# Performance work log

Measured on AMD Instinct MI355X. Metric: run time of the kernel, lower is better.

Reference implementation:

```python
import jax, jax.numpy as jnp
import numpy as np


def _gcn_conv(x, W, b, src, dst, num_nodes):
    """PyG GCNConv: linear transform, add self-loops, symmetric norm, scatter-add."""
    h = x @ W  # [N, out] - transform first (cheaper gather on small dim)
    loop = jnp.arange(num_nodes, dtype=src.dtype)
    s = jnp.concatenate([src, loop])  # sources (message senders)
    d = jnp.concatenate([dst, loop])  # targets (aggregators)
    deg = jax.ops.segment_sum(jnp.ones_like(d, dtype=h.dtype), d, num_segments=num_nodes)
    dinv = jnp.where(deg > 0, jax.lax.rsqrt(deg), 0.0)
    norm = dinv[s] * dinv[d]  # [E+N]
    msg = h[s] * norm[:, None]  # gather + scale
    out = jax.ops.segment_sum(msg, d, num_segments=num_nodes)  # scatter-add
    return out + b


def setup_inputs() -> dict:
    key = jax.random.key(0)
    k1, k2, k3, k4 = jax.random.split(key, 4)
    N, F_IN, H, C, E = 100000, 128, 16, 7, 3200000
    x = jax.random.normal(k1, (N, F_IN), dtype=jnp.float32)
    edge_index = jax.random.randint(k2, (2, E), 0, N, dtype=jnp.int64)
    W1 = jax.random.normal(k3, (F_IN, H), dtype=jnp.float32) / np.sqrt(F_IN)
    b1 = jnp.zeros((H,), dtype=jnp.float32)
    W2 = jax.random.normal(k4, (H, C), dtype=jnp.float32) / np.sqrt(H)
    b2 = jnp.zeros((C,), dtype=jnp.float32)
    return {"x": x, "edge_index": edge_index, "W1": W1, "b1": b1, "W2": W2, "b2": b2}


def reference(x, edge_index, W1, b1, W2, b2):
    N = x.shape[0]
    src, dst = edge_index[0], edge_index[1]
    h = _gcn_conv(x, W1, b1, src, dst, N)
    h = jax.nn.relu(h)
    # dropout is identity in eval mode
    h = _gcn_conv(h, W2, b2, src, dst, N)
    return jax.nn.log_softmax(h, axis=1)
```

## Files before the change

### kernel.cpp

```cpp
#include <hip/hip_runtime.h>

#define BSHIFT 7
#define BNODES 128
#define BMASK 127
#define CAP 6144
#define PT 512
#define P_EPB (PT * 16)
#define TPB 256

__device__ __forceinline__ unsigned pkbf2(float a, float b) {
    unsigned ua = __float_as_uint(a), ub = __float_as_uint(b);
    ua = (ua + 0x7fffu + ((ua >> 16) & 1u)) >> 16;
    ub = (ub + 0x7fffu + ((ub >> 16) & 1u)) >> 16;
    return ua | (ub << 16);
}
__device__ __forceinline__ float bflo(unsigned u) { return __uint_as_float(u << 16); }
__device__ __forceinline__ float bfhi(unsigned u) { return __uint_as_float(u & 0xffff0000u); }

__global__ void detect_kernel(const unsigned int* __restrict__ w, int* __restrict__ flag,
                              int* __restrict__ gcur, int nb) {
    __shared__ int any;
    if (threadIdx.x == 0) any = 0;
    __syncthreads();
    int nz = 0;
    for (int k = threadIdx.x; k < 1024; k += blockDim.x)
        if (w[2 * k + 1] != 0u) nz = 1;
    if (nz) atomicOr(&any, 1);
    for (int i = threadIdx.x; i < nb; i += blockDim.x) gcur[i] = 0;
    __syncthreads();
    if (threadIdx.x == 0) *flag = (any == 0) ? 1 : 0;
}

__global__ __launch_bounds__(PT) void fused_place_gemm_kernel(
    const void* __restrict__ ei, const int* __restrict__ flag,
    int* __restrict__ gcur, unsigned* __restrict__ pairs,
    const float* __restrict__ x, const float* __restrict__ W1,
    uint4* __restrict__ hs1u, int E, int nb, int pb, int N) {
    __shared__ alignas(16) char smem[47120];
    int tid = threadIdx.x;
    if ((int)blockIdx.x < pb) {
        int* cnt  = (int*)smem;
        int* bbs  = (int*)(smem + 4096);
        int* cur  = (int*)(smem + 8208);
        int* ssum = (int*)(smem + 12304);
        unsigned* stage = (unsigned*)(smem + 14352);
        const bool is64 = (*flag != 0);
        const long long* e64 = (const long long*)ei;
        const int* e32 = (const int*)ei;
        int e0 = blockIdx.x * P_EPB;
        int tot = E - e0; if (tot > P_EPB) tot = P_EPB;
        for (int b = tid; b < nb; b += PT) cnt[b] = 0;
        __syncthreads();
        unsigned pk[16];
        int bk[16];
#pragma unroll
        for (int k = 0; k < 16; ++k) {
            int i = tid + k * PT;
            bk[k] = -1;
            if (i < tot) {
                int e = e0 + i;
                int s, d;
                if (is64) { s = (int)e64[e]; d = (int)e64[E + e]; }
                else      { s = e32[e];      d = e32[E + e]; }
                int b = d >> BSHIFT;
                bk[k] = b;
                pk[k] = ((unsigned)s << BSHIFT) | (unsigned)(d & BMASK);
                atomicAdd(&cnt[b], 1);
            }
        }
        __syncthreads();
        int t2 = tid * 2;
        int c0 = (t2 < nb) ? cnt[t2] : 0;
        int c1 = (t2 + 1 < nb) ? cnt[t2 + 1] : 0;
        int ts = c0 + c1;
        ssum[tid] = ts;
        __syncthreads();
        for (int off = 1; off < PT; off <<= 1) {
            int v = (tid >= off) ? ssum[tid - off] : 0;
            __syncthreads();
            ssum[tid] += v;
            __syncthreads();
        }
        int excl = ssum[tid] - ts;
        if (tid == PT - 1) bbs[nb] = ssum[PT - 1];
        int gb0 = 0, gb1 = 0;
        if (t2 < nb && c0) gb0 = atomicAdd(&gcur[t2], c0);
        if (t2 + 1 < nb && c1) gb1 = atomicAdd(&gcur[t2 + 1], c1);
        if (t2 < nb)     { bbs[t2] = excl;          cnt[t2] = gb0;     cur[t2] = 0; }
        if (t2 + 1 < nb) { bbs[t2 + 1] = excl + c0; cnt[t2 + 1] = gb1; cur[t2 + 1] = 0; }
        __syncthreads();
#pragma unroll
        for (int k = 0; k < 16; ++k) {
            if (bk[k] >= 0) {
                int r = atomicAdd(&cur[bk[k]], 1);
                stage[bbs[bk[k]] + r] = pk[k];
            }
        }
        __syncthreads();
        for (int i = tid; i < tot; i += PT) {
            int lo = 0, hi = nb;
            while (hi - lo > 1) { int mid = (lo + hi) >> 1; if (bbs[mid] <= i) lo = mid; else hi = mid; }
            int slot = cnt[lo] + (i - bbs[lo]);
            if (slot < CAP) pairs[(size_t)lo * CAP + slot] = stage[i];
        }
    } else {
        float* Ws = (float*)smem;
        for (int i = tid; i < 2048; i += PT) Ws[i] = W1[i];
        __syncthreads();
        int n = ((int)blockIdx.x - pb) * PT + tid;
        if (n >= N) return;
        const float4* xp = (const float4*)(x + (size_t)n * 128);
        float a[16];
#pragma unroll
        for (int j = 0; j < 16; ++j) a[j] = 0.f;
#pragma unroll 4
        for (int k4 = 0; k4 < 32; ++k4) {
            float4 xv = xp[k4];
            const float* wr = &Ws[k4 * 64];
#pragma unroll
            for (int j = 0; j < 16; ++j) a[j] += xv.x * wr[j];
#pragma unroll
            for (int j = 0; j < 16; ++j) a[j] += xv.y * wr[16 + j];
#pragma unroll
            for (int j = 0; j < 16; ++j) a[j] += xv.z * wr[32 + j];
#pragma unroll
            for (int j = 0; j < 16; ++j) a[j] += xv.w * wr[48 + j];
        }
        uint4 u0, u1;
        u0.x = pkbf2(a[0], a[1]);   u0.y = pkbf2(a[2], a[3]);
        u0.z = pkbf2(a[4], a[5]);   u0.w = pkbf2(a[6], a[7]);
        u1.x = pkbf2(a[8], a[9]);   u1.y = pkbf2(a[10], a[11]);
        u1.z = pkbf2(a[12], a[13]); u1.w = pkbf2(a[14], a[15]);
        hs1u[(size_t)n * 2]     = u0;
        hs1u[(size_t)n * 2 + 1] = u1;
    }
}

__global__ __launch_bounds__(TPB) void csr_build_kernel(
    const unsigned* __restrict__ pairs, const int* __restrict__ gcur,
    int* __restrict__ csr, int* __restrict__ row, int* __restrict__ degA,
    const uint4* __restrict__ hs1u, uint4* __restrict__ hs1b, int N) {
    __shared__ int hist[BNODES];
    __shared__ int sc[BNODES];
    __shared__ int cur[BNODES];
    __shared__ int stage[CAP];
    int tid = threadIdx.x;
    int b = blockIdx.x;
    if (tid < BNODES) hist[tid] = 0;
    __syncthreads();
    int cnt = gcur[b]; if (cnt > CAP) cnt = CAP;
    int base = b * CAP;
    const unsigned* sl = pairs + (size_t)b * CAP;
    for (int i = tid; i < cnt; i += TPB)
        atomicAdd(&hist[sl[i] & BMASK], 1);
    __syncthreads();
    if (tid < BNODES) sc[tid] = hist[tid];
    __syncthreads();
    for (int off = 1; off < BNODES; off <<= 1) {
        int u = (tid < BNODES && tid >= off) ? sc[tid - off] : 0;
        __syncthreads();
        if (tid < BNODES) sc[tid] += u;
        __syncthreads();
    }
    if (tid < BNODES) {
        int excl = sc[tid] - hist[tid];
        sc[tid] = excl;
        cur[tid] = 0;
        int node = (b << BSHIFT) + tid;
        if (node < N) {
            row[node]  = base + excl;
            degA[node] = hist[tid];
        }
    }
    __syncthreads();
    for (int i = tid; i < cnt; i += TPB) {
        unsigned val = sl[i];
        int l = val & BMASK;
        int r = atomicAdd(&cur[l], 1);
        stage[sc[l] + r] = (int)(val >> BSHIFT);
    }
    __syncthreads();
    for (int i = tid; i < cnt; i += TPB)
        csr[base + i] = stage[i];
    {
        int ln = tid >> 1, half = tid & 1;
        int node = (b << BSHIFT) + ln;
        if (node < N) {
            float s = rsqrtf((float)(hist[ln] + 1));
            uint4 uu = hs1u[(size_t)node * 2 + half];
            uint4 o;
            o.x = pkbf2(bflo(uu.x) * s, bfhi(uu.x) * s);
            o.y = pkbf2(bflo(uu.y) * s, bfhi(uu.y) * s);
            o.z = pkbf2(bflo(uu.z) * s, bfhi(uu.z) * s);
            o.w = pkbf2(bflo(uu.w) * s, bfhi(uu.w) * s);
            hs1b[(size_t)node * 2 + half] = o;
        }
    }
}

__global__ __launch_bounds__(TPB) void agg1_kernel(
    const uint4* __restrict__ hs1b, const int* __restrict__ csr,
    const int* __restrict__ row, const int* __restrict__ degA,
    const float* __restrict__ W2, const float* __restrict__ b1,
    uint4* __restrict__ hs2b, int N) {
    __shared__ float Ws[112];
    __shared__ float bs[16];
    int tid = threadIdx.x;
    if (tid < 112) Ws[tid] = W2[tid];
    if (tid < 16) bs[tid] = b1[tid];
    __syncthreads();
    int g = blockIdx.x * TPB + tid;
    int n = g >> 3, oct = g & 7;
    int st = 0, cnt = 0;
    if (n < N) { st = row[n]; cnt = degA[n]; }
    float acc[16];
#pragma unroll
    for (int j = 0; j < 16; ++j) acc[j] = 0.f;
    int i = st + oct, end = st + cnt;
    for (; i + 8 < end; i += 16) {
        int s0 = csr[i], s1 = csr[i + 8];
        uint4 g0 = hs1b[(size_t)s0 * 2], g1 = hs1b[(size_t)s0 * 2 + 1];
        uint4 h0 = hs1b[(size_t)s1 * 2], h1 = hs1b[(size_t)s1 * 2 + 1];
        acc[0]  += bflo(g0.x) + bflo(h0.x); acc[1]  += bfhi(g0.x) + bfhi(h0.x);
        acc[2]  += bflo(g0.y) + bflo(h0.y); acc[3]  += bfhi(g0.y) + bfhi(h0.y);
        acc[4]  += bflo(g0.z) + bflo(h0.z); acc[5]  += bfhi(g0.z) + bfhi(h0.z);
        acc[6]  += bflo(g0.w) + bflo(h0.w); acc[7]  += bfhi(g0.w) + bfhi(h0.w);
        acc[8]  += bflo(g1.x) + bflo(h1.x); acc[9]  += bfhi(g1.x) + bfhi(h1.x);
        acc[10] += bflo(g1.y) + bflo(h1.y); acc[11] += bfhi(g1.y) + bfhi(h1.y);
        acc[12] += bflo(g1.z) + bflo(h1.z); acc[13] += bfhi(g1.z) + bfhi(h1.z);
        acc[14] += bflo(g1.w) + bflo(h1.w); acc[15] += bfhi(g1.w) + bfhi(h1.w);
    }
    if (i < end) {
        int s0 = csr[i];
        uint4 g0 = hs1b[(size_t)s0 * 2], g1 = hs1b[(size_t)s0 * 2 + 1];
        acc[0]  += bflo(g0.x); acc[1]  += bfhi(g0.x);
        acc[2]  += bflo(g0.y); acc[3]  += bfhi(g0.y);
        acc[4]  += bflo(g0.z); acc[5]  += bfhi(g0.z);
        acc[6]  += bflo(g0.w); acc[7]  += bfhi(g0.w);
        acc[8]  += bflo(g1.x); acc[9]  += bfhi(g1.x);
        acc[10] += bflo(g1.y); acc[11] += bfhi(g1.y);
        acc[12] += bflo(g1.z); acc[13] += bfhi(g1.z);
        acc[14] += bflo(g1.w); acc[15] += bfhi(g1.w);
    }
#pragma unroll
    for (int j = 0; j < 16; ++j) {
        acc[j] += __shfl_xor(acc[j], 1);
        acc[j] += __shfl_xor(acc[j], 2);
        acc[j] += __shfl_xor(acc[j], 4);
    }
    if (oct == 0 && n < N) {
        float sc = rsqrtf((float)(cnt + 1));
        uint4 sA = hs1b[(size_t)n * 2], sB = hs1b[(size_t)n * 2 + 1];
        float self[16] = {bflo(sA.x), bfhi(sA.x), bflo(sA.y), bfhi(sA.y),
                          bflo(sA.z), bfhi(sA.z), bflo(sA.w), bfhi(sA.w),
                          bflo(sB.x), bfhi(sB.x), bflo(sB.y), bfhi(sB.y),
                          bflo(sB.z), bfhi(sB.z), bflo(sB.w), bfhi(sB.w)};
        float v[16];
#pragma unroll
        for (int j = 0; j < 16; ++j)
            v[j] = fmaxf(0.f, sc * (acc[j] + self[j]) + bs[j]);
        float h[7];
#pragma unroll
        for (int j = 0; j < 7; ++j) h[j] = 0.f;
#pragma unroll
        for (int k = 0; k < 16; ++k)
#pragma unroll
            for (int j = 0; j < 7; ++j) h[j] += v[k] * Ws[k * 7 + j];
        uint4 u;
        u.x = pkbf2(h[0] * sc, h[1] * sc);
        u.y = pkbf2(h[2] * sc, h[3] * sc);
        u.z = pkbf2(h[4] * sc, h[5] * sc);
        u.w = pkbf2(h[6] * sc, 0.f);
        hs2b[n] = u;
    }
}

__global__ __launch_bounds__(TPB) void agg2_kernel(
    const uint4* __restrict__ hs2b, const int* __restrict__ csr,
    const int* __restrict__ row, const int* __restrict__ degA,
    const float* __restrict__ b2, float* __restrict__ out, int N) {
    __shared__ float bs[8];
    if (threadIdx.x < 7) bs[threadIdx.x] = b2[threadIdx.x];
    __syncthreads();
    int g = blockIdx.x * TPB + threadIdx.x;
    int n = g >> 3, oct = g & 7;
    int st = 0, cnt = 0;
    if (n < N) { st = row[n]; cnt = degA[n]; }
    float acc[7];
#pragma unroll
    for (int j = 0; j < 7; ++j) acc[j] = 0.f;
    int i = st + oct, end = st + cnt;
    for (; i + 8 < end; i += 16) {
        int s0 = csr[i], s1 = csr[i + 8];
        uint4 q = hs2b[s0];
        uint4 r = hs2b[s1];
        acc[0] += bflo(q.x) + bflo(r.x); acc[1] += bfhi(q.x) + bfhi(r.x);
        acc[2] += bflo(q.y) + bflo(r.y); acc[3] += bfhi(q.y) + bfhi(r.y);
        acc[4] += bflo(q.z) + bflo(r.z); acc[5] += bfhi(q.z) + bfhi(r.z);
        acc[6] += bflo(q.w) + bflo(r.w);
    }
    if (i < end) {
        uint4 q = hs2b[csr[i]];
        acc[0] += bflo(q.x); acc[1] += bfhi(q.x);
        acc[2] += bflo(q.y); acc[3] += bfhi(q.y);
        acc[4] += bflo(q.z); acc[5] += bfhi(q.z);
        acc[6] += bflo(q.w);
    }
#pragma unroll
    for (int j = 0; j < 7; ++j) {
        acc[j] += __shfl_xor(acc[j], 1);
        acc[j] += __shfl_xor(acc[j], 2);
        acc[j] += __shfl_xor(acc[j], 4);
    }
    if (oct == 0 && n < N) {
        float sc = rsqrtf((float)(cnt + 1));
        uint4 q = hs2b[n];
        float self[7] = {bflo(q.x), bfhi(q.x), bflo(q.y), bfhi(q.y),
                         bflo(q.z), bfhi(q.z), bflo(q.w)};
        float v[7];
#pragma unroll
        for (int j = 0; j < 7; ++j)
            v[j] = sc * (acc[j] + self[j]) + bs[j];
        float m = v[0];
#pragma unroll
        for (int j = 1; j < 7; ++j) m = fmaxf(m, v[j]);
        float ssum = 0.f;
#pragma unroll
        for (int j = 0; j < 7; ++j) ssum += __expf(v[j] - m);
        float l = m + __logf(ssum);
        float* op = out + (size_t)n * 7;
#pragma unroll
        for (int j = 0; j < 7; ++j) op[j] = v[j] - l;
    }
}

extern "C" void kernel_launch(void* const* d_in, const int* in_sizes, int n_in,
                              void* d_out, int out_size, void* d_ws, size_t ws_size,
                              hipStream_t stream) {
    const float* x  = (const float*)d_in[0];
    const void*  ei = d_in[1];
    const float* W1 = (const float*)d_in[2];
    const float* b1 = (const float*)d_in[3];
    const float* W2 = (const float*)d_in[4];
    const float* b2 = (const float*)d_in[5];
    float* out = (float*)d_out;

    const int Hh  = in_sizes[3];
    const int Fin = in_sizes[2] / Hh;
    const int N   = in_sizes[0] / Fin;
    const long long twoE = in_sizes[1];
    const int E = (int)(twoE / 2);
    const int nb = (N + BNODES - 1) >> BSHIFT;
    (void)n_in; (void)out_size; (void)ws_size;

    char* p = (char*)d_ws;
    auto alloc = [&](size_t bytes) {
        char* r = p;
        p += (bytes + 63) & ~(size_t)63;
        return r;
    };
    int*      flag  = (int*)alloc(sizeof(int));
    int*      gcur  = (int*)alloc(sizeof(int) * (size_t)nb);
    unsigned* pairs = (unsigned*)alloc(sizeof(unsigned) * (size_t)nb * CAP);
    int*      csr   = (int*)alloc(sizeof(int) * (size_t)nb * CAP);
    int*      rowA  = (int*)alloc(sizeof(int) * (size_t)N);
    int*      degA  = (int*)alloc(sizeof(int) * (size_t)N);
    uint4*    hs1u  = (uint4*)alloc(32 * (size_t)N);
    uint4*    hs1b  = (uint4*)alloc(32 * (size_t)N);
    uint4*    hs2b  = (uint4*)alloc(16 * (size_t)N);

    const int pb = (E + P_EPB - 1) / P_EPB;
    const int gb = (N + PT - 1) / PT;

    detect_kernel<<<1, 256, 0, stream>>>((const unsigned int*)ei, flag, gcur, nb);
    fused_place_gemm_kernel<<<pb + gb, PT, 0, stream>>>(
        ei, flag, gcur, pairs, x, W1, hs1u, E, nb, pb, N);
    csr_build_kernel<<<nb, TPB, 0, stream>>>(pairs, gcur, csr, rowA, degA, hs1u, hs1b, N);
    agg1_kernel<<<(8 * N + TPB - 1) / TPB, TPB, 0, stream>>>(hs1b, csr, rowA, degA, W2, b1, hs2b, N);
    agg2_kernel<<<(8 * N + TPB - 1) / TPB, TPB, 0, stream>>>(hs2b, csr, rowA, degA, b2, out, N);
}
```

Before: 113.1 us.

## Fold dtype detection into placement kernel, double edges per thread, use wave-shuffle scan

Drops the separate detect kernel: each placement block now checks itself whether the edge indices are int64, and gcur is zeroed with a memset. Each thread now handles 32 edges instead of 16, which halves the number of placement blocks and the global atomics per bucket. The 512-step LDS scan with barriers is replaced by a wave-level shuffle scan plus a small cross-wave fixup. In exchange, shared memory grows to about 78KB and register pressure rises, which may reduce occupancy, and every block repeats the dtype probe.

```diff
diff --git a/kernel.cpp b/kernel.cpp
--- a/kernel.cpp
+++ b/kernel.cpp
@@ -5,8 +5,11 @@
 #define BMASK 127
 #define CAP 6144
 #define PT 512
-#define P_EPB (PT * 16)
+#define EPT 32
+#define P_EPB (PT * EPT)
 #define TPB 256
+
+#define SM_BYTES 77904
 
 __device__ __forceinline__ unsigned pkbf2(float a, float b) {
     unsigned ua = __float_as_uint(a), ub = __float_as_uint(b);
@@ -17,44 +20,39 @@
 __device__ __forceinline__ float bflo(unsigned u) { return __uint_as_float(u << 16); }
 __device__ __forceinline__ float bfhi(unsigned u) { return __uint_as_float(u & 0xffff0000u); }
 
-__global__ void detect_kernel(const unsigned int* __restrict__ w, int* __restrict__ flag,
-                              int* __restrict__ gcur, int nb) {
-    __shared__ int any;
-    if (threadIdx.x == 0) any = 0;
-    __syncthreads();
-    int nz = 0;
-    for (int k = threadIdx.x; k < 1024; k += blockDim.x)
-        if (w[2 * k + 1] != 0u) nz = 1;
-    if (nz) atomicOr(&any, 1);
-    for (int i = threadIdx.x; i < nb; i += blockDim.x) gcur[i] = 0;
-    __syncthreads();
-    if (threadIdx.x == 0) *flag = (any == 0) ? 1 : 0;
-}
-
 __global__ __launch_bounds__(PT) void fused_place_gemm_kernel(
-    const void* __restrict__ ei, const int* __restrict__ flag,
+    const void* __restrict__ ei,
     int* __restrict__ gcur, unsigned* __restrict__ pairs,
     const float* __restrict__ x, const float* __restrict__ W1,
     uint4* __restrict__ hs1u, int E, int nb, int pb, int N) {
-    __shared__ alignas(16) char smem[47120];
+    __shared__ alignas(16) char smem[SM_BYTES];
     int tid = threadIdx.x;
     if ((int)blockIdx.x < pb) {
         int* cnt  = (int*)smem;
         int* bbs  = (int*)(smem + 4096);
         int* cur  = (int*)(smem + 8208);
         int* ssum = (int*)(smem + 12304);
-        unsigned* stage = (unsigned*)(smem + 14352);
-        const bool is64 = (*flag != 0);
+        unsigned* stage = (unsigned*)(smem + 12368);
+
+        for (int b = tid; b < 1024; b += PT) cnt[b] = 0;
+        if (tid == 0) ssum[15] = 0;
+        const unsigned* w = (const unsigned*)ei;
+        int nz = 0;
+        for (int k = tid; k < 1024; k += PT)
+            if (w[2 * k + 1]) nz = 1;
+        __syncthreads();
+        if (nz) atomicOr(&ssum[15], 1);
+        __syncthreads();
+        const bool is64 = (ssum[15] == 0);
         const long long* e64 = (const long long*)ei;
         const int* e32 = (const int*)ei;
-        int e0 = blockIdx.x * P_EPB;
+        int e0 = (int)blockIdx.x * P_EPB;
         int tot = E - e0; if (tot > P_EPB) tot = P_EPB;
-        for (int b = tid; b < nb; b += PT) cnt[b] = 0;
-        __syncthreads();
-        unsigned pk[16];
-        int bk[16];
-#pragma unroll
-        for (int k = 0; k < 16; ++k) {
+
+        unsigned pk[EPT];
+        int bk[EPT];
+#pragma unroll
+        for (int k = 0; k < EPT; ++k) {
             int i = tid + k * PT;
             bk[k] = -1;
             if (i < tot) {
@@ -70,19 +68,24 @@
         }
         __syncthreads();
         int t2 = tid * 2;
-        int c0 = (t2 < nb) ? cnt[t2] : 0;
-        int c1 = (t2 + 1 < nb) ? cnt[t2 + 1] : 0;
+        int c0 = cnt[t2], c1 = cnt[t2 + 1];
         int ts = c0 + c1;
-        ssum[tid] = ts;
-        __syncthreads();
-        for (int off = 1; off < PT; off <<= 1) {
-            int v = (tid >= off) ? ssum[tid - off] : 0;
-            __syncthreads();
-            ssum[tid] += v;
-            __syncthreads();
-        }
-        int excl = ssum[tid] - ts;
-        if (tid == PT - 1) bbs[nb] = ssum[PT - 1];
+        int v = ts;
+#pragma unroll
+        for (int off = 1; off < 64; off <<= 1) {
+            int u = __shfl_up(v, off);
+            if ((tid & 63) >= off) v += u;
+        }
+        if ((tid & 63) == 63) ssum[tid >> 6] = v;
+        __syncthreads();
+        if (tid == 0) {
+            int r = 0;
+#pragma unroll
+            for (int wv = 0; wv < 8; ++wv) { int xx = ssum[wv]; ssum[wv] = r; r += xx; }
+        }
+        __syncthreads();
+        int excl = v - ts + ssum[tid >> 6];
+        if (tid == 0) bbs[nb] = tot;
         int gb0 = 0, gb1 = 0;
         if (t2 < nb && c0) gb0 = atomicAdd(&gcur[t2], c0);
         if (t2 + 1 < nb && c1) gb1 = atomicAdd(&gcur[t2 + 1], c1);
@@ -90,7 +93,7 @@
         if (t2 + 1 < nb) { bbs[t2 + 1] = excl + c0; cnt[t2 + 1] = gb1; cur[t2 + 1] = 0; }
         __syncthreads();
 #pragma unroll
-        for (int k = 0; k < 16; ++k) {
+        for (int k = 0; k < EPT; ++k) {
             if (bk[k] >= 0) {
                 int r = atomicAdd(&cur[bk[k]], 1);
                 stage[bbs[bk[k]] + r] = pk[k];
@@ -359,7 +362,6 @@
         p += (bytes + 63) & ~(size_t)63;
         return r;
     };
-    int*      flag  = (int*)alloc(sizeof(int));
     int*      gcur  = (int*)alloc(sizeof(int) * (size_t)nb);
     unsigned* pairs = (unsigned*)alloc(sizeof(unsigned) * (size_t)nb * CAP);
     int*      csr   = (int*)alloc(sizeof(int) * (size_t)nb * CAP);
@@ -372,9 +374,9 @@
     const int pb = (E + P_EPB - 1) / P_EPB;
     const int gb = (N + PT - 1) / PT;
 
-    detect_kernel<<<1, 256, 0, stream>>>((const unsigned int*)ei, flag, gcur, nb);
+    hipMemsetAsync(gcur, 0, sizeof(int) * (size_t)nb, stream);
     fused_place_gemm_kernel<<<pb + gb, PT, 0, stream>>>(
-        ei, flag, gcur, pairs, x, W1, hs1u, E, nb, pb, N);
+        ei, gcur, pairs, x, W1, hs1u, E, nb, pb, N);
     csr_build_kernel<<<nb, TPB, 0, stream>>>(pairs, gcur, csr, rowA, degA, hs1u, hs1b, N);
     agg1_kernel<<<(8 * N + TPB - 1) / TPB, TPB, 0, stream>>>(hs1b, csr, rowA, degA, W2, b1, hs2b, N);
     agg2_kernel<<<(8 * N + TPB - 1) / TPB, TPB, 0, stream>>>(hs2b, csr, rowA, degA, b2, out, N);
```

Result: slower. 122.4 us (+8.2%).
